# Kernel tuning notes

Measured on AMD Instinct MI355X. Metric: run time of the kernel, lower is better.

Reference implementation:

```python
import jax, jax.numpy as jnp
import numpy as np

LAYER_SHAPES = [(256, 64, 56, 56), (256, 128, 28, 28), (256, 256, 14, 14), (256, 512, 7, 7)]
NUM_REF = 2000


def _lid_layer(ref, q, k):
    """MLE LID estimate (Ma et al.) per query row.
    ref: [R, C] reference activations; q: [B, C] pooled query activations.
    """
    # Euclidean cdist via the expansion ||q||^2 - 2 q.ref^T + ||ref||^2
    d2 = (jnp.sum(q * q, axis=1, keepdims=True)
          - 2.0 * (q @ ref.T)
          + jnp.sum(ref * ref, axis=1)[None, :])            # [B, R]
    d = jnp.sqrt(jnp.maximum(d2, 0.0))
    # smallest k+1 distances, drop the nearest (mirrors sorted[:,1:k+1])
    neg_topk = jax.lax.top_k(-d, k + 1)[0]                   # descending in -d => ascending d
    dk = -neg_topk[:, 1:k + 1]                               # [B, k], ascending
    # LID = -k / sum_i log(d_i / d_k)
    return -k / jnp.sum(jnp.log(dk / dk[:, -1:]), axis=1)    # [B]


def setup_inputs() -> dict:
    key = jax.random.key(0)
    ks = jax.random.split(key, 12)
    inp = {}
    for i, shp in enumerate(LAYER_SHAPES):
        inp[f"feat{i}"] = jax.random.normal(ks[i], shp, dtype=jnp.float32)
        inp[f"ref{i}"] = jax.random.normal(ks[4 + i], (NUM_REF, shp[1]), dtype=jnp.float32)
    inp["reg_w"] = jax.random.normal(ks[8], (1, 4), dtype=jnp.float32)
    inp["reg_b"] = jax.random.normal(ks[9], (1,), dtype=jnp.float32)
    inp["k"] = 20
    return inp


def reference(feat0, feat1, feat2, feat3, ref0, ref1, ref2, ref3, reg_w, reg_b, k):
    feats = [feat0, feat1, feat2, feat3]
    refs = [ref0, ref1, ref2, ref3]
    lid_scores = []
    for f, r in zip(feats, refs):
        fq = jnp.mean(f.reshape(f.shape[0], f.shape[1], -1), axis=2)  # [B, C]
        lid_scores.append(_lid_layer(r, fq, k))
    lid_feat = jnp.stack(lid_scores, axis=1)                 # [B, num_layers]
    logit = lid_feat @ reg_w.T + reg_b                        # [B, 1]
    return jax.nn.sigmoid(logit)[:, 0]
```

## Files before the change

kernel.cpp:

```cpp
#include <hip/hip_runtime.h>
#include <cmath>

#define WS_FQ_OFF      0u
#define WS_R2_OFF      245760u
#define WS_LID_OFF     253760u
#define WS_G_OFF       262144u
#define G_LAYER_STRIDE 512000u
#define NREF           2000

__global__ __launch_bounds__(256) void pool_r2_kernel(const float* __restrict__ f0,
                                                      const float* __restrict__ f1,
                                                      const float* __restrict__ f2,
                                                      const float* __restrict__ f3,
                                                      const float* __restrict__ r0,
                                                      const float* __restrict__ r1,
                                                      const float* __restrict__ r2p,
                                                      const float* __restrict__ r3,
                                                      float* __restrict__ fq_all,
                                                      float* __restrict__ r2_all) {
    int blk = blockIdx.x;
    int t = threadIdx.x;
    int w = t >> 6, lane = t & 63;

    if (blk < 4096) {
        size_t row = (size_t)blk * 4 + w;
        const float4* p4 = (const float4*)(f0 + row * 3136);
        float s = 0.f;
        {
            float4 v[6];
            #pragma unroll
            for (int j = 0; j < 6; ++j) v[j] = p4[lane + j * 64];
            #pragma unroll
            for (int j = 0; j < 6; ++j) s += (v[j].x + v[j].y) + (v[j].z + v[j].w);
            #pragma unroll
            for (int j = 0; j < 6; ++j) v[j] = p4[lane + (j + 6) * 64];
            #pragma unroll
            for (int j = 0; j < 6; ++j) s += (v[j].x + v[j].y) + (v[j].z + v[j].w);
        }
        if (lane < 16) { float4 v = p4[768 + lane]; s += (v.x + v.y) + (v.z + v.w); }
        #pragma unroll
        for (int off = 32; off; off >>= 1) s += __shfl_down(s, off, 64);
        if (lane == 0) fq_all[row] = s * (1.0f / 3136.f);
    } else if (blk < 12288) {
        size_t row = (size_t)(blk - 4096) * 4 + w;
        const float4* p4 = (const float4*)(f1 + row * 784);
        float s = 0.f;
        {
            float4 v[3];
            #pragma unroll
            for (int j = 0; j < 3; ++j) v[j] = p4[lane + j * 64];
            #pragma unroll
            for (int j = 0; j < 3; ++j) s += (v[j].x + v[j].y) + (v[j].z + v[j].w);
        }
        if (lane < 4) { float4 v = p4[192 + lane]; s += (v.x + v.y) + (v.z + v.w); }
        #pragma unroll
        for (int off = 32; off; off >>= 1) s += __shfl_down(s, off, 64);
        if (lane == 0) fq_all[16384 + row] = s * (1.0f / 784.f);
    } else if (blk < 12544) {
        int row = (blk - 12288) * 256 + t;
        const float4* p4 = (const float4*)(f2 + (size_t)row * 196);
        float s = 0.f;
        #pragma unroll 1
        for (int base = 0; base < 48; base += 6) {
            float4 v[6];
            #pragma unroll
            for (int j = 0; j < 6; ++j) v[j] = p4[base + j];
            #pragma unroll
            for (int j = 0; j < 6; ++j) s += (v[j].x + v[j].y) + (v[j].z + v[j].w);
        }
        { float4 v = p4[48]; s += (v.x + v.y) + (v.z + v.w); }
        fq_all[49152 + row] = s * (1.0f / 196.f);
    } else if (blk < 13056) {
        int row = (blk - 12544) * 256 + t;
        const float* p = f3 + (size_t)row * 49;
        float s = 0.f;
        #pragma unroll 1
        for (int base = 0; base < 48; base += 6) {
            float v[6];
            #pragma unroll
            for (int j = 0; j < 6; ++j) v[j] = p[base + j];
            #pragma unroll
            for (int j = 0; j < 6; ++j) s += v[j];
        }
        s += p[48];
        fq_all[114688 + row] = s * (1.0f / 49.f);
    } else {
        int rb = blk - 13056;
        int layer = rb / 500;
        int r = (rb % 500) * 4 + w;
        if (r >= NREF) return;
        const float* rp; int C;
        switch (layer) {
            case 0:  rp = r0;  C = 64;  break;
            case 1:  rp = r1;  C = 128; break;
            case 2:  rp = r2p; C = 256; break;
            default: rp = r3;  C = 512; break;
        }
        const float4* rowp = (const float4*)(rp + (size_t)r * C);
        int n4 = C >> 2;
        float s = 0.f;
        for (int i = lane; i < n4; i += 64) {
            float4 v = rowp[i];
            s += v.x*v.x + v.y*v.y + v.z*v.z + v.w*v.w;
        }
        #pragma unroll
        for (int off = 32; off; off >>= 1) s += __shfl_down(s, off, 64);
        if (lane == 0) r2_all[layer * NREF + r] = s;
    }
}

#define BM 64
#define BN 64
#define BK 32
#define LDT 68
__global__ __launch_bounds__(256) void gemm_all(const float* __restrict__ fq_all,
                                                const float* __restrict__ ref0,
                                                const float* __restrict__ ref1,
                                                const float* __restrict__ ref2,
                                                const float* __restrict__ ref3,
                                                float* __restrict__ G) {
    __shared__ __align__(16) float As[BK * LDT];
    __shared__ __align__(16) float Bs[BK * LDT];
    int layer = blockIdx.z;
    const float* B; int K;
    switch (layer) {
        case 0:  B = ref0; K = 64;  break;
        case 1:  B = ref1; K = 128; break;
        case 2:  B = ref2; K = 256; break;
        default: B = ref3; K = 512; break;
    }
    const int fqo[4] = {0, 16384, 49152, 114688};
    const float* A = fq_all + fqo[layer];
    float* Gout = G + (size_t)layer * G_LAYER_STRIDE;

    int t = threadIdx.x;
    int tq = t & 15, tr = t >> 4;
    int m0 = blockIdx.x * BM;
    int n0 = blockIdx.y * BN;
    int row0 = t >> 3;
    int kc4  = t & 7;
    float acc[4][4] = {};

    for (int k0 = 0; k0 < K; k0 += BK) {
        #pragma unroll
        for (int half = 0; half < 2; ++half) {
            int row = row0 + half * 32;
            float4 av = *(const float4*)(A + (size_t)(m0 + row) * K + k0 + kc4 * 4);
            int brow = n0 + row;
            float4 bv = make_float4(0.f, 0.f, 0.f, 0.f);
            if (brow < NREF) bv = *(const float4*)(B + (size_t)brow * K + k0 + kc4 * 4);
            As[(kc4*4 + 0) * LDT + row] = av.x;
            As[(kc4*4 + 1) * LDT + row] = av.y;
            As[(kc4*4 + 2) * LDT + row] = av.z;
            As[(kc4*4 + 3) * LDT + row] = av.w;
            Bs[(kc4*4 + 0) * LDT + row] = bv.x;
            Bs[(kc4*4 + 1) * LDT + row] = bv.y;
            Bs[(kc4*4 + 2) * LDT + row] = bv.z;
            Bs[(kc4*4 + 3) * LDT + row] = bv.w;
        }
        __syncthreads();
        #pragma unroll
        for (int kk = 0; kk < BK; ++kk) {
            float4 a = *(const float4*)&As[kk * LDT + tq * 4];
            float4 b = *(const float4*)&Bs[kk * LDT + tr * 4];
            acc[0][0] += a.x*b.x; acc[0][1] += a.x*b.y; acc[0][2] += a.x*b.z; acc[0][3] += a.x*b.w;
            acc[1][0] += a.y*b.x; acc[1][1] += a.y*b.y; acc[1][2] += a.y*b.z; acc[1][3] += a.y*b.w;
            acc[2][0] += a.z*b.x; acc[2][1] += a.z*b.y; acc[2][2] += a.z*b.z; acc[2][3] += a.z*b.w;
            acc[3][0] += a.w*b.x; acc[3][1] += a.w*b.y; acc[3][2] += a.w*b.z; acc[3][3] += a.w*b.w;
        }
        __syncthreads();
    }

    int rbase = n0 + tr * 4;
    if (rbase < NREF) {
        #pragma unroll
        for (int i = 0; i < 4; ++i) {
            float4 o = make_float4(acc[i][0], acc[i][1], acc[i][2], acc[i][3]);
            *(float4*)(Gout + (size_t)(m0 + tq*4 + i) * NREF + rbase) = o;
        }
    }
}

__global__ __launch_bounds__(256) void topk_lid_kernel(const float* __restrict__ fq_all,
                                                       const float* __restrict__ G_all,
                                                       const float* __restrict__ r2_all,
                                                       float* __restrict__ lid,
                                                       const int* __restrict__ kptr) {
    __shared__ __align__(16) float d2s[NREF];
    __shared__ unsigned hist[2048];
    __shared__ float redq[4], redm[4], redl[4];
    __shared__ unsigned long long red8[4];
    __shared__ int sh_B, sh_cbelow, sh_cnt;
    __shared__ float sh_dmin;

    const int Cs[4]   = {64, 128, 256, 512};
    const int fqo[4]  = {0, 16384, 49152, 114688};

    int b = blockIdx.x, layer = blockIdx.y;
    int t = threadIdx.x;
    int lane = t & 63, w = t >> 6;
    int k = kptr[0];
    if (k + 1 > NREF) k = NREF - 1;
    unsigned K1 = (unsigned)(k + 1);
    int C = Cs[layer];
    const float* fq = fq_all + fqo[layer] + (size_t)b * C;
    const float* Gb = G_all + (size_t)layer * G_LAYER_STRIDE + (size_t)b * NREF;
    const float* r2 = r2_all + layer * NREF;
    const float INF = __uint_as_float(0x7f800000u);

    for (int i = t; i < 2048; i += 256) hist[i] = 0u;
    if (t == 0) sh_cnt = 0;
    float s = 0.f;
    for (int c = t; c < C; c += 256) { float v = fq[c]; s += v * v; }
    #pragma unroll
    for (int off = 32; off; off >>= 1) s += __shfl_down(s, off, 64);
    if (lane == 0) redq[w] = s;
    __syncthreads();
    float q2 = redq[0] + redq[1] + redq[2] + redq[3];

    float minv = INF;
    for (int i = t; i < NREF / 4; i += 256) {
        float4 g = *(const float4*)(Gb + i * 4);
        float4 rr = *(const float4*)(r2 + i * 4);
        float d0 = q2 - 2.f * g.x + rr.x; d0 = d0 > 0.f ? d0 : 0.f;
        float d1 = q2 - 2.f * g.y + rr.y; d1 = d1 > 0.f ? d1 : 0.f;
        float d2_ = q2 - 2.f * g.z + rr.z; d2_ = d2_ > 0.f ? d2_ : 0.f;
        float d3 = q2 - 2.f * g.w + rr.w; d3 = d3 > 0.f ? d3 : 0.f;
        *(float4*)(d2s + i * 4) = make_float4(d0, d1, d2_, d3);
        atomicAdd(&hist[__float_as_uint(d0) >> 20], 1u);
        atomicAdd(&hist[__float_as_uint(d1) >> 20], 1u);
        atomicAdd(&hist[__float_as_uint(d2_) >> 20], 1u);
        atomicAdd(&hist[__float_as_uint(d3) >> 20], 1u);
        minv = fminf(minv, fminf(fminf(d0, d1), fminf(d2_, d3)));
    }
    #pragma unroll
    for (int off = 32; off; off >>= 1) minv = fminf(minv, __shfl_down(minv, off, 64));
    if (lane == 0) redm[w] = minv;
    __syncthreads();

    if (t < 64) {
        unsigned p = 0;
        int base = t * 32;
        #pragma unroll 4
        for (int i = 0; i < 32; ++i) p += hist[base + i];
        unsigned cum = p;
        #pragma unroll
        for (int off = 1; off < 64; off <<= 1) {
            unsigned o = __shfl_up(cum, off, 64);
            if (t >= off) cum += o;
        }
        unsigned excl = cum - p;
        if (excl < K1 && K1 <= cum) {
            unsigned run = excl;
            int binB = base;
            for (int i = 0; i < 32; ++i) {
                unsigned c = hist[base + i];
                if (run + c >= K1) { binB = base + i; break; }
                run += c;
            }
            sh_B = binB;
            sh_cbelow = (int)run;
        }
        if (t == 0) sh_dmin = fminf(fminf(redm[0], redm[1]), fminf(redm[2], redm[3]));
    }
    __syncthreads();

    int B = sh_B;
    float* cand = (float*)hist;
    float lsum = 0.f;
    for (int i = t; i < NREF; i += 256) {
        float v = d2s[i];
        int bin = (int)(__float_as_uint(v) >> 20);
        if (bin < B) {
            lsum += logf(v);
        } else if (bin == B) {
            int pos = atomicAdd(&sh_cnt, 1);
            cand[pos] = v;
        }
    }
    #pragma unroll
    for (int off = 32; off; off >>= 1) lsum += __shfl_down(lsum, off, 64);
    if (lane == 0) redl[w] = lsum;
    __syncthreads();

    int cnt = sh_cnt;
    int m = (int)K1 - sh_cbelow;
    if (cnt <= 64) {
        if (t < 64) {
            float mv = (t < cnt) ? cand[t] : INF;
            float csum = 0.f, dk = 0.f;
            for (int it = 0; it < m; ++it) {
                float x = mv;
                #pragma unroll
                for (int off = 32; off; off >>= 1) x = fminf(x, __shfl_xor(x, off, 64));
                csum += logf(x);
                dk = x;
                unsigned long long ball = __ballot(mv == x);
                int src = __ffsll(ball) - 1;
                if (t == src) mv = INF;
            }
            if (t == 0) {
                float lsum_tot = redl[0] + redl[1] + redl[2] + redl[3];
                float denom = 0.5f * (lsum_tot + csum - logf(sh_dmin) - (float)k * logf(dk));
                lid[b * 4 + layer] = -(float)k / denom;
            }
        }
    } else {
        float csum = 0.f, dk = 0.f;
        for (int it = 0; it < m; ++it) {
            unsigned long long best = ~0ull;
            for (int i = t; i < cnt; i += 256) {
                unsigned long long key =
                    ((unsigned long long)__float_as_uint(cand[i]) << 32) | (unsigned)i;
                if (key < best) best = key;
            }
            #pragma unroll
            for (int off = 32; off; off >>= 1) {
                unsigned long long o = __shfl_down(best, off, 64);
                if (o < best) best = o;
            }
            if (lane == 0) red8[w] = best;
            __syncthreads();
            unsigned long long mm = red8[0];
            #pragma unroll
            for (int ww = 1; ww < 4; ++ww) if (red8[ww] < mm) mm = red8[ww];
            float v = __uint_as_float((unsigned)(mm >> 32));
            if (t == 0) {
                csum += logf(v);
                dk = v;
                cand[(int)(mm & 0xffffffffu)] = INF;
            }
            __syncthreads();
        }
        if (t == 0) {
            float lsum_tot = redl[0] + redl[1] + redl[2] + redl[3];
            float denom = 0.5f * (lsum_tot + csum - logf(sh_dmin) - (float)k * logf(dk));
            lid[b * 4 + layer] = -(float)k / denom;
        }
    }
}

__global__ __launch_bounds__(256) void head_kernel(const float* __restrict__ lid,
                                                   const float* __restrict__ w,
                                                   const float* __restrict__ bias,
                                                   float* __restrict__ out) {
    int b = threadIdx.x;
    float acc = bias[0];
    #pragma unroll
    for (int l = 0; l < 4; ++l) acc += lid[b * 4 + l] * w[l];
    out[b] = 1.f / (1.f + expf(-acc));
}

extern "C" void kernel_launch(void* const* d_in, const int* in_sizes, int n_in,
                              void* d_out, int out_size, void* d_ws, size_t ws_size,
                              hipStream_t stream) {
    const float* feat[4] = {(const float*)d_in[0], (const float*)d_in[2],
                            (const float*)d_in[4], (const float*)d_in[6]};
    const float* ref[4]  = {(const float*)d_in[1], (const float*)d_in[3],
                            (const float*)d_in[5], (const float*)d_in[7]};
    const float* reg_w = (const float*)d_in[8];
    const float* reg_b = (const float*)d_in[9];
    const int*   kptr  = (const int*)d_in[10];

    float* ws     = (float*)d_ws;
    float* fq_all = ws + WS_FQ_OFF;
    float* r2_all = ws + WS_R2_OFF;
    float* lid    = ws + WS_LID_OFF;
    float* G      = ws + WS_G_OFF;

    pool_r2_kernel<<<15056, 256, 0, stream>>>(
        feat[0], feat[1], feat[2], feat[3],
        ref[0], ref[1], ref[2], ref[3],
        fq_all, r2_all);

    gemm_all<<<dim3(256 / BM, (NREF + BN - 1) / BN, 4), 256, 0, stream>>>(
        fq_all, ref[0], ref[1], ref[2], ref[3], G);

    topk_lid_kernel<<<dim3(256, 4), 256, 0, stream>>>(fq_all, G, r2_all, lid, kptr);

    head_kernel<<<1, 256, 0, stream>>>(lid, reg_w, reg_b, (float*)d_out);
}
```

Baseline: 483.0 us.

## Use grid-stride persistent blocks with wave-per-row pooling in pool kernel

The pooling/ref-norm kernel now launches 2304 blocks that grid-stride over rows, where before it launched one block per few rows (15056 blocks). Layers 2 and 3 now reduce each row with a full wavefront and shuffles, where before one thread summed a whole row with strided, uncoalesced loads. The aim is to cut block launch overhead and make the small-row layers use coalesced memory access. The cost is fewer blocks in flight, which may lower memory-level parallelism on the large first layer. The layer-3 rows also use only 49 of 64 lanes.

Measured after the change: 488.9 us. About the same (+1.2%).

```diff
diff --git a/kernel.cpp b/kernel.cpp
--- a/kernel.cpp
+++ b/kernel.cpp
@@ -22,90 +22,90 @@
     int t = threadIdx.x;
     int w = t >> 6, lane = t & 63;
 
-    if (blk < 4096) {
-        size_t row = (size_t)blk * 4 + w;
-        const float4* p4 = (const float4*)(f0 + row * 3136);
-        float s = 0.f;
-        {
-            float4 v[6];
-            #pragma unroll
-            for (int j = 0; j < 6; ++j) v[j] = p4[lane + j * 64];
-            #pragma unroll
-            for (int j = 0; j < 6; ++j) s += (v[j].x + v[j].y) + (v[j].z + v[j].w);
-            #pragma unroll
-            for (int j = 0; j < 6; ++j) v[j] = p4[lane + (j + 6) * 64];
-            #pragma unroll
-            for (int j = 0; j < 6; ++j) s += (v[j].x + v[j].y) + (v[j].z + v[j].w);
-        }
-        if (lane < 16) { float4 v = p4[768 + lane]; s += (v.x + v.y) + (v.z + v.w); }
-        #pragma unroll
-        for (int off = 32; off; off >>= 1) s += __shfl_down(s, off, 64);
-        if (lane == 0) fq_all[row] = s * (1.0f / 3136.f);
-    } else if (blk < 12288) {
-        size_t row = (size_t)(blk - 4096) * 4 + w;
-        const float4* p4 = (const float4*)(f1 + row * 784);
-        float s = 0.f;
-        {
-            float4 v[3];
-            #pragma unroll
-            for (int j = 0; j < 3; ++j) v[j] = p4[lane + j * 64];
-            #pragma unroll
-            for (int j = 0; j < 3; ++j) s += (v[j].x + v[j].y) + (v[j].z + v[j].w);
-        }
-        if (lane < 4) { float4 v = p4[192 + lane]; s += (v.x + v.y) + (v.z + v.w); }
-        #pragma unroll
-        for (int off = 32; off; off >>= 1) s += __shfl_down(s, off, 64);
-        if (lane == 0) fq_all[16384 + row] = s * (1.0f / 784.f);
-    } else if (blk < 12544) {
-        int row = (blk - 12288) * 256 + t;
-        const float4* p4 = (const float4*)(f2 + (size_t)row * 196);
-        float s = 0.f;
-        #pragma unroll 1
-        for (int base = 0; base < 48; base += 6) {
-            float4 v[6];
-            #pragma unroll
-            for (int j = 0; j < 6; ++j) v[j] = p4[base + j];
-            #pragma unroll
-            for (int j = 0; j < 6; ++j) s += (v[j].x + v[j].y) + (v[j].z + v[j].w);
-        }
-        { float4 v = p4[48]; s += (v.x + v.y) + (v.z + v.w); }
-        fq_all[49152 + row] = s * (1.0f / 196.f);
-    } else if (blk < 13056) {
-        int row = (blk - 12544) * 256 + t;
-        const float* p = f3 + (size_t)row * 49;
-        float s = 0.f;
-        #pragma unroll 1
-        for (int base = 0; base < 48; base += 6) {
-            float v[6];
-            #pragma unroll
-            for (int j = 0; j < 6; ++j) v[j] = p[base + j];
-            #pragma unroll
-            for (int j = 0; j < 6; ++j) s += v[j];
-        }
-        s += p[48];
-        fq_all[114688 + row] = s * (1.0f / 49.f);
+    if (blk < 512) {
+        int gw = blk * 4 + w;
+        for (int it = 0; it < 8; ++it) {
+            size_t row = (size_t)gw + (size_t)it * 2048;
+            const float4* p4 = (const float4*)(f0 + row * 3136);
+            float s = 0.f;
+            {
+                float4 v[6];
+                #pragma unroll
+                for (int j = 0; j < 6; ++j) v[j] = p4[lane + j * 64];
+                #pragma unroll
+                for (int j = 0; j < 6; ++j) s += (v[j].x + v[j].y) + (v[j].z + v[j].w);
+                #pragma unroll
+                for (int j = 0; j < 6; ++j) v[j] = p4[lane + (j + 6) * 64];
+                #pragma unroll
+                for (int j = 0; j < 6; ++j) s += (v[j].x + v[j].y) + (v[j].z + v[j].w);
+            }
+            if (lane < 16) { float4 v = p4[768 + lane]; s += (v.x + v.y) + (v.z + v.w); }
+            #pragma unroll
+            for (int off = 32; off; off >>= 1) s += __shfl_down(s, off, 64);
+            if (lane == 0) fq_all[row] = s * (1.0f / 3136.f);
+        }
+    } else if (blk < 1024) {
+        int gw = (blk - 512) * 4 + w;
+        for (int it = 0; it < 16; ++it) {
+            size_t row = (size_t)gw + (size_t)it * 2048;
+            const float4* p4 = (const float4*)(f1 + row * 784);
+            float4 v0 = p4[lane];
+            float4 v1 = p4[lane + 64];
+            float4 v2 = p4[lane + 128];
+            float s = (v0.x + v0.y) + (v0.z + v0.w)
+                    + (v1.x + v1.y) + (v1.z + v1.w)
+                    + (v2.x + v2.y) + (v2.z + v2.w);
+            if (lane < 4) { float4 vt = p4[192 + lane]; s += (vt.x + vt.y) + (vt.z + vt.w); }
+            #pragma unroll
+            for (int off = 32; off; off >>= 1) s += __shfl_down(s, off, 64);
+            if (lane == 0) fq_all[16384 + row] = s * (1.0f / 784.f);
+        }
+    } else if (blk < 1536) {
+        int gw = (blk - 1024) * 4 + w;
+        for (int it = 0; it < 32; ++it) {
+            size_t row = (size_t)gw + (size_t)it * 2048;
+            const float4* p4 = (const float4*)(f2 + row * 196);
+            float s = 0.f;
+            if (lane < 49) { float4 v = p4[lane]; s = (v.x + v.y) + (v.z + v.w); }
+            #pragma unroll
+            for (int off = 32; off; off >>= 1) s += __shfl_down(s, off, 64);
+            if (lane == 0) fq_all[49152 + row] = s * (1.0f / 196.f);
+        }
+    } else if (blk < 2048) {
+        int gw = (blk - 1536) * 4 + w;
+        for (int it = 0; it < 64; ++it) {
+            size_t row = (size_t)gw + (size_t)it * 2048;
+            const float* p = f3 + row * 49;
+            float s = (lane < 49) ? p[lane] : 0.f;
+            #pragma unroll
+            for (int off = 32; off; off >>= 1) s += __shfl_down(s, off, 64);
+            if (lane == 0) fq_all[114688 + row] = s * (1.0f / 49.f);
+        }
     } else {
-        int rb = blk - 13056;
-        int layer = rb / 500;
-        int r = (rb % 500) * 4 + w;
-        if (r >= NREF) return;
-        const float* rp; int C;
-        switch (layer) {
-            case 0:  rp = r0;  C = 64;  break;
-            case 1:  rp = r1;  C = 128; break;
-            case 2:  rp = r2p; C = 256; break;
-            default: rp = r3;  C = 512; break;
-        }
-        const float4* rowp = (const float4*)(rp + (size_t)r * C);
-        int n4 = C >> 2;
-        float s = 0.f;
-        for (int i = lane; i < n4; i += 64) {
-            float4 v = rowp[i];
-            s += v.x*v.x + v.y*v.y + v.z*v.z + v.w*v.w;
-        }
-        #pragma unroll
-        for (int off = 32; off; off >>= 1) s += __shfl_down(s, off, 64);
-        if (lane == 0) r2_all[layer * NREF + r] = s;
+        int gw = (blk - 2048) * 4 + w;
+        for (int it = 0; it < 8; ++it) {
+            int u = gw + it * 1024;
+            if (u >= 8000) break;
+            int layer = u / 2000;
+            int r = u - layer * 2000;
+            const float* rp; int C;
+            switch (layer) {
+                case 0:  rp = r0;  C = 64;  break;
+                case 1:  rp = r1;  C = 128; break;
+                case 2:  rp = r2p; C = 256; break;
+                default: rp = r3;  C = 512; break;
+            }
+            const float4* rowp = (const float4*)(rp + (size_t)r * C);
+            int n4 = C >> 2;
+            float s = 0.f;
+            for (int i = lane; i < n4; i += 64) {
+                float4 v = rowp[i];
+                s += v.x*v.x + v.y*v.y + v.z*v.z + v.w*v.w;
+            }
+            #pragma unroll
+            for (int off = 32; off; off >>= 1) s += __shfl_down(s, off, 64);
+            if (lane == 0) r2_all[layer * NREF + r] = s;
+        }
     }
 }
 
@@ -368,7 +368,7 @@
     float* lid    = ws + WS_LID_OFF;
     float* G      = ws + WS_G_OFF;
 
-    pool_r2_kernel<<<15056, 256, 0, stream>>>(
+    pool_r2_kernel<<<2304, 256, 0, stream>>>(
         feat[0], feat[1], feat[2], feat[3],
         ref[0], ref[1], ref[2], ref[3],
         fq_all, r2_all);
```
